# Optimization experiments

Measured on AMD Instinct MI355X. Metric: run time of the kernel, lower is better.

## Reference

```python
import jax, jax.numpy as jnp
import numpy as np

B, T, D, K, DEPTH = 8, 1024, 128, 64, 1


def _rel_ids(T, k):
    # relative_mat_id[i, j] = clamp(k + j - i, 0, 2k)
    base = jnp.arange(k, k + T)[None, :] - jnp.arange(T)[:, None]
    return jnp.clip(base, 0, 2 * k)  # [T, T] int32


def setup_inputs() -> dict:
    key = jax.random.key(0)
    ks = jax.random.split(key, 13)
    s = 1.0 / np.sqrt(D)
    return {
        "x": jax.random.normal(ks[0], (B, T, D), dtype=jnp.float32),
        "W0": jax.random.normal(ks[1], (D, D), dtype=jnp.float32) * s,
        "b0": jnp.zeros((D,), dtype=jnp.float32),
        "Wq": jax.random.normal(ks[2], (D, D), dtype=jnp.float32) * s,
        "bq": jnp.zeros((D,), dtype=jnp.float32),
        "Wk": jax.random.normal(ks[3], (D, D), dtype=jnp.float32) * s,
        "bk": jnp.zeros((D,), dtype=jnp.float32),
        "Wv": jax.random.normal(ks[4], (D, D), dtype=jnp.float32) * s,
        "bv": jnp.zeros((D,), dtype=jnp.float32),
        "W1": jax.random.normal(ks[5], (D, D), dtype=jnp.float32) * s,
        "b1": jnp.zeros((D,), dtype=jnp.float32),
        "pe_key": jax.random.normal(ks[6], (2 * K + 1, D), dtype=jnp.float32) * np.sqrt(2.0 / (2 * K + 1)),
        "pe_value": jax.random.normal(ks[7], (2 * K + 1, D), dtype=jnp.float32) * np.sqrt(2.0 / (2 * K + 1)),
    }


def reference(x, W0, b0, Wq, bq, Wk, bk, Wv, bv, W1, b1, pe_key, pe_value):
    Tlen = x.shape[1]
    ids = _rel_ids(Tlen, K)                     # [T, T]
    rpr_key = pe_key[ids]                       # [T, T, D]
    rpr_value = pe_value[ids]                   # [T, T, D]

    hs = jax.nn.relu(x @ W0 + b0)               # fc0 (dropout = eval identity)
    for _ in range(DEPTH):
        q = jnp.tanh(hs @ Wq + bq)
        k = jnp.tanh(hs @ Wk + bk)
        v = jnp.tanh(hs @ Wv + bv)
        a = jnp.einsum("bid,bjd->bij", q, k)
        a = a + jnp.einsum("ijd,bid->bij", rpr_key, q)
        a = jax.nn.softmax(a, axis=2)
        c = jnp.einsum("bij,bjd->bid", a, v)
        c = c + jnp.einsum("bij,ijd->bid", a, rpr_value)
        hs = jax.nn.relu(c @ W1 + b1)
    return hs
```

## Files before the change

### kernel.cpp

```cpp
#include <hip/hip_runtime.h>


#define TT 1024
#define DD 128
#define NB 8
#define SJH 1160

typedef _Float16 f16;
typedef __attribute__((ext_vector_type(8))) _Float16 f16x8;
typedef __attribute__((ext_vector_type(4))) _Float16 f16x4;
typedef __attribute__((ext_vector_type(4))) float f32x4;

static __device__ inline float fast_tanh(float x) {
    float xc = fminf(fmaxf(x, -12.f), 12.f);
    float e = __expf(2.f * xc);
    return (e - 1.f) / (e + 1.f);
}

__global__ __launch_bounds__(256) void prep_misc(
        const float* __restrict__ W0, const float* __restrict__ Wq,
        const float* __restrict__ Wk, const float* __restrict__ Wv,
        const float* __restrict__ W1, const float* __restrict__ PEK,
        const float* __restrict__ PEV, f16* __restrict__ wt,
        char* __restrict__ pekimg, char* __restrict__ pevimg) {
    const int blk = blockIdx.x, t = threadIdx.x;
    if (blk < 5) {
        const float* W = blk == 0 ? W0 : blk == 1 ? Wq : blk == 2 ? Wk
                       : blk == 3 ? Wv : W1;
        f16* o = wt + (size_t)blk * 16384;
        for (int it = 0; it < 64; it++) {
            int idx = t + 256 * it;
            int n = idx >> 7, k2 = idx & 127;
            o[n * 128 + k2] = (f16)W[k2 * 128 + n];
        }
    } else if (blk == 5) {
        for (int it = 0; it < 64; it++) {
            int idx = t + 256 * it;
            int m = idx >> 7, d = idx & 127;
            char* dst = pekimg + (m >> 6) * 16384 + (m & 63) * 256
                      + ((2 * d) ^ ((m & 7) << 4));
            *(f16*)dst = (f16)PEK[m * 128 + d];
        }
    } else if (blk == 6) {
        for (int it = 0; it < 64; it++) {
            int idx = t + 256 * it;
            int m = idx >> 7, d = idx & 127;
            char* dst = pevimg + (m >> 6) * 16384 + d * 128
                      + ((2 * (m & 63)) ^ ((d & 7) << 4));
            *(f16*)dst = (f16)PEV[m * 128 + d];
        }
    }
}

template<int ACT, int INF32, int OUTF32>
__global__ __launch_bounds__(256) void gemm16(const void* __restrict__ Xv,
        const f16* __restrict__ WT, const float* __restrict__ Bv,
        void* __restrict__ Yv) {
    __shared__ __align__(16) char lds[40960];
    char* xs = lds;
    char* wl = lds + 8192;
    const int t = threadIdx.x, wv = t >> 6, l = t & 63;
    const int r0 = blockIdx.x * 32;

    {
        const char* src = (const char*)WT;
        #pragma unroll
        for (int i = 0; i < 8; i++) {
            int a = t * 128 + i * 16;
            uint4 d = *(const uint4*)(src + a);
            *(uint4*)(wl + (a ^ (((a >> 8) & 7) << 4))) = d;
        }
    }
    if (INF32) {
        const float* X = (const float*)Xv + (size_t)r0 * 128;
        #pragma unroll
        for (int i = 0; i < 2; i++) {
            f32x4 a0 = *(const f32x4*)(X + t * 16 + i * 8);
            f32x4 a1 = *(const f32x4*)(X + t * 16 + i * 8 + 4);
            f16x8 h;
            h[0]=(f16)a0[0]; h[1]=(f16)a0[1]; h[2]=(f16)a0[2]; h[3]=(f16)a0[3];
            h[4]=(f16)a1[0]; h[5]=(f16)a1[1]; h[6]=(f16)a1[2]; h[7]=(f16)a1[3];
            int a = t * 32 + i * 16;
            *(f16x8*)(xs + (a ^ (((a >> 8) & 7) << 4))) = h;
        }
    } else {
        const char* X = (const char*)Xv + (size_t)r0 * 256;
        #pragma unroll
        for (int i = 0; i < 2; i++) {
            int a = t * 32 + i * 16;
            uint4 d = *(const uint4*)(X + a);
            *(uint4*)(xs + (a ^ (((a >> 8) & 7) << 4))) = d;
        }
    }
    __syncthreads();

    f32x4 acc[2][2] = {};
    #pragma unroll
    for (int c = 0; c < 4; c++) {
        f16x8 af[2], bf[2];
        #pragma unroll
        for (int it = 0; it < 2; it++) {
            int row = it * 16 + (l & 15);
            int a = (row << 8) + (c << 6) + ((l >> 4) << 4);
            af[it] = *(const f16x8*)(xs + (a ^ ((row & 7) << 4)));
        }
        #pragma unroll
        for (int nt = 0; nt < 2; nt++) {
            int n = wv * 32 + nt * 16 + (l & 15);
            int a = (n << 8) + (c << 6) + ((l >> 4) << 4);
            bf[nt] = *(const f16x8*)(wl + (a ^ ((n & 7) << 4)));
        }
        #pragma unroll
        for (int it = 0; it < 2; it++)
            #pragma unroll
            for (int nt = 0; nt < 2; nt++)
                acc[it][nt] = __builtin_amdgcn_mfma_f32_16x16x32_f16(
                        af[it], bf[nt], acc[it][nt], 0, 0, 0);
    }

    #pragma unroll
    for (int it = 0; it < 2; it++)
        #pragma unroll
        for (int nt = 0; nt < 2; nt++) {
            int n = wv * 32 + nt * 16 + (l & 15);
            float bb = Bv[n];
            #pragma unroll
            for (int r = 0; r < 4; r++) {
                int i = it * 16 + (l >> 4) * 4 + r;
                float v = acc[it][nt][r] + bb;
                v = (ACT == 0) ? fmaxf(v, 0.f) : fast_tanh(v);
                if (OUTF32) ((float*)Yv)[(size_t)(r0 + i) * 128 + n] = v;
                else        ((f16*)Yv)[(size_t)(r0 + i) * 128 + n] = (f16)v;
            }
        }
}

__global__ __launch_bounds__(256) void gemm_qkv(const f16* __restrict__ X,
        const f16* __restrict__ wt, const float* __restrict__ bq,
        const float* __restrict__ bk, const float* __restrict__ bv,
        f16* __restrict__ q16, char* __restrict__ kimg, char* __restrict__ vimg) {
    __shared__ __align__(16) char lds[40960];
    char* xs = lds;
    char* wl = lds + 8192;
    const int t = threadIdx.x, wv = t >> 6, l = t & 63;
    const int sel = blockIdx.x % 3;
    const int r0 = (blockIdx.x / 3) * 32;
    const f16* WT = wt + (size_t)(sel + 1) * 16384;
    const float* Bv = sel == 0 ? bq : sel == 1 ? bk : bv;

    {
        const char* src = (const char*)WT;
        #pragma unroll
        for (int i = 0; i < 8; i++) {
            int a = t * 128 + i * 16;
            uint4 d = *(const uint4*)(src + a);
            *(uint4*)(wl + (a ^ (((a >> 8) & 7) << 4))) = d;
        }
    }
    {
        const char* Xc = (const char*)X + (size_t)r0 * 256;
        #pragma unroll
        for (int i = 0; i < 2; i++) {
            int a = t * 32 + i * 16;
            uint4 d = *(const uint4*)(Xc + a);
            *(uint4*)(xs + (a ^ (((a >> 8) & 7) << 4))) = d;
        }
    }
    __syncthreads();

    f32x4 acc[2][2] = {};
    #pragma unroll
    for (int c = 0; c < 4; c++) {
        f16x8 af[2], bf[2];
        #pragma unroll
        for (int it = 0; it < 2; it++) {
            int row = it * 16 + (l & 15);
            int a = (row << 8) + (c << 6) + ((l >> 4) << 4);
            af[it] = *(const f16x8*)(xs + (a ^ ((row & 7) << 4)));
        }
        #pragma unroll
        for (int nt = 0; nt < 2; nt++) {
            int n = wv * 32 + nt * 16 + (l & 15);
            int a = (n << 8) + (c << 6) + ((l >> 4) << 4);
            bf[nt] = *(const f16x8*)(wl + (a ^ ((n & 7) << 4)));
        }
        #pragma unroll
        for (int it = 0; it < 2; it++)
            #pragma unroll
            for (int nt = 0; nt < 2; nt++)
                acc[it][nt] = __builtin_amdgcn_mfma_f32_16x16x32_f16(
                        af[it], bf[nt], acc[it][nt], 0, 0, 0);
    }

    if (sel == 0) {
        #pragma unroll
        for (int it = 0; it < 2; it++)
            #pragma unroll
            for (int nt = 0; nt < 2; nt++) {
                int n = wv * 32 + nt * 16 + (l & 15);
                float bb = Bv[n];
                #pragma unroll
                for (int r = 0; r < 4; r++) {
                    int i = it * 16 + (l >> 4) * 4 + r;
                    q16[(size_t)(r0 + i) * 128 + n] = (f16)fast_tanh(acc[it][nt][r] + bb);
                }
            }
    } else if (sel == 1) {
        __syncthreads();
        f16* ts = (f16*)lds;
        #pragma unroll
        for (int it = 0; it < 2; it++)
            #pragma unroll
            for (int nt = 0; nt < 2; nt++) {
                int n = wv * 32 + nt * 16 + (l & 15);
                float bb = Bv[n];
                #pragma unroll
                for (int r = 0; r < 4; r++) {
                    int i = it * 16 + (l >> 4) * 4 + r;
                    ts[i * 128 + n] = (f16)fast_tanh(acc[it][nt][r] + bb);
                }
            }
        __syncthreads();
        #pragma unroll
        for (int half = 0; half < 2; half++) {
            int row = (t >> 4) + half * 16, seg = t & 15;
            int jg = r0 + row, jp = jg & 63;
            char* dst = kimg + (size_t)((jg >> 10) * 16 + ((jg & 1023) >> 6)) * 16384
                      + jp * 256 + ((seg * 16) ^ ((jp & 7) << 4));
            *(f16x8*)dst = *(const f16x8*)&ts[row * 128 + seg * 8];
        }
    } else {
        #pragma unroll
        for (int it = 0; it < 2; it++)
            #pragma unroll
            for (int nt = 0; nt < 2; nt++) {
                int n = wv * 32 + nt * 16 + (l & 15);
                float bb = Bv[n];
                f16x4 h;
                #pragma unroll
                for (int r = 0; r < 4; r++)
                    h[r] = (f16)fast_tanh(acc[it][nt][r] + bb);
                int jb = r0 + it * 16 + ((l >> 4) << 2);
                char* dst = vimg + (size_t)((jb >> 10) * 16 + ((jb & 1023) >> 6)) * 16384
                          + n * 128 + ((2 * (jb & 63)) ^ ((n & 7) << 4));
                *(f16x4*)dst = h;
            }
    }
}

#define ISSUE(src, bi) do {                                                      \
    const char* _g = (src) + t * 16;                                             \
    char* _d = BUF + (bi) * 16384 + t * 16;                                      \
    __builtin_amdgcn_global_load_lds(                                            \
        (const __attribute__((address_space(1))) unsigned*)_g,                   \
        (__attribute__((address_space(3))) unsigned*)_d, 16, 0, 0);              \
    __builtin_amdgcn_global_load_lds(                                            \
        (const __attribute__((address_space(1))) unsigned*)(_g + 8192),          \
        (__attribute__((address_space(3))) unsigned*)(_d + 8192), 16, 0, 0);     \
} while (0)

__global__ __launch_bounds__(512) void attn_v5(
        const f16* __restrict__ q16, const char* __restrict__ kimg,
        const char* __restrict__ pekimg, const char* __restrict__ vimg,
        const char* __restrict__ pevimg, const float* __restrict__ PEK,
        const float* __restrict__ PEV, f16* __restrict__ c16) {
    extern __shared__ __align__(16) char sm5[];
    f16*   S   = (f16*)sm5;
    char*  BUF = sm5 + 74240;
    f16*   QB  = (f16*)(sm5 + 74240 + 65536);
    float* LR  = (float*)(sm5 + 74240 + 65536 + 8448);

    const int t = threadIdx.x, wv = t >> 6, l = t & 63;
    const int lr = l & 15, lg = l >> 4;
    const int b = blockIdx.x & 7;
    const int i0 = (blockIdx.x >> 3) << 5;
    const int it = wv & 1, jsub = wv >> 1;

    f16x8 qf[4];
    {
        const f16* qb = q16 + (size_t)(b * 1024 + i0 + it * 16 + lr) * 128 + lg * 8;
        #pragma unroll
        for (int c = 0; c < 4; c++) qf[c] = *(const f16x8*)(qb + c * 32);
    }

    const char* kbase = kimg + (size_t)b * 16 * 16384;
    const char* vbase = vimg + (size_t)b * 16 * 16384;

    ISSUE(kbase, 0);
    ISSUE(kbase + 16384, 1);

    for (int ch = 0; ch < 18; ch++) {
        if (ch < 14)      ISSUE(kbase + (size_t)(ch + 2) * 16384, (ch + 2) & 3);
        else if (ch < 16) ISSUE(pekimg + (size_t)(ch - 14) * 16384, (ch + 2) & 3);
        else              ISSUE(vbase + (size_t)(ch - 16) * 16384, (ch + 2) & 3);
        asm volatile("s_waitcnt vmcnt(4)" ::: "memory");
        __builtin_amdgcn_s_barrier();
        __builtin_amdgcn_sched_barrier(0);

        const char* kb = BUF + (ch & 3) * 16384;
        const int jp = jsub * 16 + lr;
        f32x4 acc = {0.f, 0.f, 0.f, 0.f};
        #pragma unroll
        for (int c = 0; c < 4; c++) {
            f16x8 kf = *(const f16x8*)(kb + jp * 256 + ((c * 64 + lg * 16) ^ ((jp & 7) << 4)));
            acc = __builtin_amdgcn_mfma_f32_16x16x32_f16(kf, qf[c], acc, 0, 0, 0);
        }
        f16x4 h = {(f16)acc[0], (f16)acc[1], (f16)acc[2], (f16)acc[3]};
        *(f16x4*)&S[(it * 16 + lr) * SJH + ch * 64 + jsub * 16 + lg * 4] = h;
    }
    asm volatile("s_waitcnt lgkmcnt(0)" ::: "memory");
    __builtin_amdgcn_s_barrier();
    __builtin_amdgcn_sched_barrier(0);

    {
        const int row = t >> 4, l16 = t & 15;
        const int ig = i0 + row;
        f16* srow = S + row * SJH;
        f16* qrow = QB + row * 132;

        float qp;
        {
            const f16* qr = q16 + (size_t)(b * 1024 + ig) * 128 + l16 * 8;
            const float* pr = PEK + 128 * 128 + l16 * 8;
            f16x8 qv = *(const f16x8*)qr;
            float s = 0.f;
            #pragma unroll
            for (int e = 0; e < 8; e++) s += (float)qv[e] * pr[e];
            #pragma unroll
            for (int off = 8; off; off >>= 1) s += __shfl_xor(s, off, 64);
            qp = s;
        }
        for (int mm = l16; mm < 128; mm += 16) {
            qrow[mm] = srow[1024 + mm];
            srow[1024 + mm] = (f16)0.f;
        }
        if (l16 == 0) qrow[128] = (f16)qp;
        const float qlo = (float)qrow[0], qhi = qp;

        float lmax = -3.0e38f;
        #pragma unroll
        for (int kk = 0; kk < 8; kk++) {
            int j0 = kk * 128 + l16 * 8;
            f16x8 sv = *(const f16x8*)(srow + j0);
            #pragma unroll
            for (int e = 0; e < 8; e++) {
                int idd = 64 + j0 + e - ig;
                float qv = (idd <= 0) ? qlo : (idd >= 128 ? qhi : (float)qrow[idd]);
                lmax = fmaxf(lmax, (float)sv[e] + qv);
            }
        }
        #pragma unroll
        for (int off = 8; off; off >>= 1) lmax = fmaxf(lmax, __shfl_xor(lmax, off, 64));

        float lsum = 0.f, s0 = 0.f, s1 = 0.f;
        #pragma unroll
        for (int kk = 0; kk < 8; kk++) {
            int j0 = kk * 128 + l16 * 8;
            f16x8 sv = *(const f16x8*)(srow + j0);
            f16x8 pv;
            #pragma unroll
            for (int e = 0; e < 8; e++) {
                int idd = 64 + j0 + e - ig;
                float qv = (idd <= 0) ? qlo : (idd >= 128 ? qhi : (float)qrow[idd]);
                float p = __expf((float)sv[e] + qv - lmax);
                pv[e] = (f16)p;
                lsum += p;
                if (idd <= 0)        s0 += p;
                else if (idd >= 128) s1 += p;
                else                 srow[1024 + idd] = (f16)p;
            }
            *(f16x8*)(srow + j0) = pv;
        }
        #pragma unroll
        for (int off = 8; off; off >>= 1) {
            lsum += __shfl_xor(lsum, off, 64);
            s0   += __shfl_xor(s0,   off, 64);
            s1   += __shfl_xor(s1,   off, 64);
        }
        if (l16 == 0) {
            srow[1024] = (f16)s0;
            srow[1152] = (f16)s1;
            LR[row] = lsum;
        }
    }
    asm volatile("s_waitcnt lgkmcnt(0)" ::: "memory");
    __builtin_amdgcn_s_barrier();
    __builtin_amdgcn_sched_barrier(0);

    f32x4 cacc[2] = {};
    for (int ch = 0; ch < 18; ch++) {
        if (ch < 14) {
            ISSUE(vbase + (size_t)(ch + 2) * 16384, (ch + 4) & 3);
            asm volatile("s_waitcnt vmcnt(4)" ::: "memory");
        } else if (ch < 16) {
            ISSUE(pevimg + (size_t)(ch - 14) * 16384, (ch + 4) & 3);
            asm volatile("s_waitcnt vmcnt(4)" ::: "memory");
        } else if (ch == 16) {
            asm volatile("s_waitcnt vmcnt(2)" ::: "memory");
        } else {
            asm volatile("s_waitcnt vmcnt(0)" ::: "memory");
        }
        __builtin_amdgcn_s_barrier();
        __builtin_amdgcn_sched_barrier(0);

        const char* vb = BUF + ((ch + 2) & 3) * 16384;
        const int dp = wv * 16 + lr;
        #pragma unroll
        for (int c2 = 0; c2 < 2; c2++) {
            f16x8 vf = *(const f16x8*)(vb + dp * 128 + ((c2 * 64 + lg * 16) ^ ((dp & 7) << 4)));
            #pragma unroll
            for (int i2 = 0; i2 < 2; i2++) {
                f16x8 pf = *(const f16x8*)&S[(i2 * 16 + lr) * SJH + ch * 64 + c2 * 32 + lg * 8];
                cacc[i2] = __builtin_amdgcn_mfma_f32_16x16x32_f16(vf, pf, cacc[i2], 0, 0, 0);
            }
        }
    }

    #pragma unroll
    for (int i2 = 0; i2 < 2; i2++) {
        const int irow = i2 * 16 + lr;
        const float w128 = (float)S[irow * SJH + 1152];
        const float rin = 1.f / LR[irow];
        const float* pvr = PEV + 128 * 128;
        f16x4 h;
        #pragma unroll
        for (int r = 0; r < 4; r++) {
            int d = wv * 16 + lg * 4 + r;
            h[r] = (f16)((cacc[i2][r] + w128 * pvr[d]) * rin);
        }
        *(f16x4*)(c16 + (size_t)(b * 1024 + i0 + irow) * 128 + wv * 16 + lg * 4) = h;
    }
}


extern "C" void kernel_launch(void* const* d_in, const int* in_sizes, int n_in,
                              void* d_out, int out_size, void* d_ws, size_t ws_size,
                              hipStream_t stream) {
    const float* x   = (const float*)d_in[0];
    const float* W0  = (const float*)d_in[1];
    const float* b0  = (const float*)d_in[2];
    const float* Wq  = (const float*)d_in[3];
    const float* bq  = (const float*)d_in[4];
    const float* Wk  = (const float*)d_in[5];
    const float* bk  = (const float*)d_in[6];
    const float* Wv  = (const float*)d_in[7];
    const float* bv  = (const float*)d_in[8];
    const float* W1  = (const float*)d_in[9];
    const float* b1  = (const float*)d_in[10];
    const float* pek = (const float*)d_in[11];
    const float* pev = (const float*)d_in[12];
    float* out = (float*)d_out;

    const size_t NTD = (size_t)NB * TT * DD;
    f16* hs16 = (f16*)d_ws;
    f16* q16  = hs16 + NTD;
    f16* c16  = q16 + NTD;
    f16* wt   = c16 + NTD;
    char* kimg   = (char*)(wt + 5 * 16384);
    char* vimg   = kimg + (size_t)8 * 16 * 16384;
    char* pekimg = vimg + (size_t)8 * 16 * 16384;
    char* pevimg = pekimg + 32768;

    const int SMEM_ATTN = 74240 + 65536 + 8448 + 128;
    hipFuncSetAttribute(reinterpret_cast<const void*>(attn_v5),
                        hipFuncAttributeMaxDynamicSharedMemorySize, SMEM_ATTN);

    hipLaunchKernelGGL(prep_misc, dim3(7), dim3(256), 0, stream,
                       W0, Wq, Wk, Wv, W1, pek, pev, wt, pekimg, pevimg);
    hipLaunchKernelGGL((gemm16<0,1,0>), dim3(256), dim3(256), 0, stream,
                       x, wt, b0, hs16);
    hipLaunchKernelGGL(gemm_qkv, dim3(768), dim3(256), 0, stream,
                       hs16, wt, bq, bk, bv, q16, kimg, vimg);
    hipLaunchKernelGGL(attn_v5, dim3(256), dim3(512), SMEM_ATTN, stream,
                       q16, kimg, pekimg, vimg, pevimg, pek, pev, c16);
    hipLaunchKernelGGL((gemm16<0,0,1>), dim3(256), dim3(256), 0, stream,
                       c16, wt + 4 * 16384, b1, out);
}
```

Before: 57.98 us.

## Fuse fc0 into QKV kernel and fc1 into attention, use 128-row K/V chunks

The fc0 GEMM is folded into a single kernel that keeps the relu'd hidden state in LDS and computes Q, K and V from it, so the hs16 round trip through global memory and one launch are gone. The W1 output projection plus relu is fused into the attention epilogue, which removes the c16 buffer and the final GEMM launch. The K/V image layout moves to 128-row 32KB chunks with double buffering and full vmcnt(0) waits, replacing the 4-deep 16KB pipeline. The trade-off is more serial work per block (four dependent GEMMs in the QKV kernel, 258 blocks instead of 768) and shallower load prefetch in attention.

```diff
diff --git a/kernel.cpp b/kernel.cpp
--- a/kernel.cpp
+++ b/kernel.cpp
@@ -17,62 +17,83 @@
     return (e - 1.f) / (e + 1.f);
 }
 
-__global__ __launch_bounds__(256) void prep_misc(
+__global__ __launch_bounds__(256) void prep_w(
         const float* __restrict__ W0, const float* __restrict__ Wq,
         const float* __restrict__ Wk, const float* __restrict__ Wv,
-        const float* __restrict__ W1, const float* __restrict__ PEK,
-        const float* __restrict__ PEV, f16* __restrict__ wt,
-        char* __restrict__ pekimg, char* __restrict__ pevimg) {
+        const float* __restrict__ W1, f16* __restrict__ wt) {
     const int blk = blockIdx.x, t = threadIdx.x;
-    if (blk < 5) {
-        const float* W = blk == 0 ? W0 : blk == 1 ? Wq : blk == 2 ? Wk
-                       : blk == 3 ? Wv : W1;
-        f16* o = wt + (size_t)blk * 16384;
-        for (int it = 0; it < 64; it++) {
-            int idx = t + 256 * it;
-            int n = idx >> 7, k2 = idx & 127;
-            o[n * 128 + k2] = (f16)W[k2 * 128 + n];
-        }
-    } else if (blk == 5) {
-        for (int it = 0; it < 64; it++) {
-            int idx = t + 256 * it;
-            int m = idx >> 7, d = idx & 127;
-            char* dst = pekimg + (m >> 6) * 16384 + (m & 63) * 256
-                      + ((2 * d) ^ ((m & 7) << 4));
-            *(f16*)dst = (f16)PEK[m * 128 + d];
-        }
-    } else if (blk == 6) {
-        for (int it = 0; it < 64; it++) {
-            int idx = t + 256 * it;
-            int m = idx >> 7, d = idx & 127;
-            char* dst = pevimg + (m >> 6) * 16384 + d * 128
-                      + ((2 * (m & 63)) ^ ((d & 7) << 4));
-            *(f16*)dst = (f16)PEV[m * 128 + d];
-        }
+    const float* W = blk == 0 ? W0 : blk == 1 ? Wq : blk == 2 ? Wk
+                   : blk == 3 ? Wv : W1;
+    f16* o = wt + (size_t)blk * 16384;
+    for (int it = 0; it < 64; it++) {
+        int idx = t + 256 * it;
+        int n = idx >> 7, k2 = idx & 127;
+        o[n * 128 + k2] = (f16)W[k2 * 128 + n];
     }
 }
 
-template<int ACT, int INF32, int OUTF32>
-__global__ __launch_bounds__(256) void gemm16(const void* __restrict__ Xv,
-        const f16* __restrict__ WT, const float* __restrict__ Bv,
-        void* __restrict__ Yv) {
-    __shared__ __align__(16) char lds[40960];
-    char* xs = lds;
-    char* wl = lds + 8192;
+#define STAGEW(s) do { const char* _src = (const char*)(wt + (size_t)(s) * 16384); \
+    _Pragma("unroll") for (int _i = 0; _i < 8; _i++) { \
+        int _a = t * 128 + _i * 16; uint4 _d = *(const uint4*)(_src + _a); \
+        *(uint4*)(wl + (_a ^ (((_a >> 8) & 7) << 4))) = _d; } } while (0)
+
+#define ZACC() do { _Pragma("unroll") for (int _i = 0; _i < 2; _i++) \
+    _Pragma("unroll") for (int _j = 0; _j < 2; _j++) \
+        acc[_i][_j] = (f32x4){0.f, 0.f, 0.f, 0.f}; } while (0)
+
+#define GEMMCORE(SRC) do { \
+    _Pragma("unroll") for (int _c = 0; _c < 4; _c++) { \
+        f16x8 _af[2], _bf[2]; \
+        _Pragma("unroll") for (int _it = 0; _it < 2; _it++) { \
+            int _row = _it * 16 + (l & 15); \
+            int _a = (_row << 8) + (_c << 6) + ((l >> 4) << 4); \
+            _af[_it] = *(const f16x8*)((SRC) + (_a ^ ((_row & 7) << 4))); } \
+        _Pragma("unroll") for (int _nt = 0; _nt < 2; _nt++) { \
+            int _n = wv * 32 + _nt * 16 + (l & 15); \
+            int _a = (_n << 8) + (_c << 6) + ((l >> 4) << 4); \
+            _bf[_nt] = *(const f16x8*)(wl + (_a ^ ((_n & 7) << 4))); } \
+        _Pragma("unroll") for (int _it = 0; _it < 2; _it++) \
+        _Pragma("unroll") for (int _nt = 0; _nt < 2; _nt++) \
+            acc[_it][_nt] = __builtin_amdgcn_mfma_f32_16x16x32_f16( \
+                    _af[_it], _bf[_nt], acc[_it][_nt], 0, 0, 0); } } while (0)
+
+__global__ __launch_bounds__(256) void fused_qkv(
+        const float* __restrict__ x, const f16* __restrict__ wt,
+        const float* __restrict__ b0, const float* __restrict__ bq,
+        const float* __restrict__ bk, const float* __restrict__ bv,
+        const float* __restrict__ PEK, const float* __restrict__ PEV,
+        f16* __restrict__ q16, char* __restrict__ kimg,
+        char* __restrict__ vimg, char* __restrict__ pekimg,
+        char* __restrict__ pevimg) {
+    __shared__ __align__(16) char lds[49152];
+    char* xs  = lds;
+    char* hsl = lds + 8192;
+    char* wl  = lds + 16384;
     const int t = threadIdx.x, wv = t >> 6, l = t & 63;
-    const int r0 = blockIdx.x * 32;
-
-    {
-        const char* src = (const char*)WT;
-        #pragma unroll
-        for (int i = 0; i < 8; i++) {
-            int a = t * 128 + i * 16;
-            uint4 d = *(const uint4*)(src + a);
-            *(uint4*)(wl + (a ^ (((a >> 8) & 7) << 4))) = d;
-        }
-    }
-    if (INF32) {
-        const float* X = (const float*)Xv + (size_t)r0 * 128;
+    const int blk = blockIdx.x;
+
+    if (blk >= 256) {
+        if (blk == 256) {
+            for (int it = 0; it < 64; it++) {
+                int idx = t + 256 * it;
+                int m = idx >> 7, d = idx & 127;
+                *(f16*)(pekimg + m * 256 + ((2 * d) ^ ((m & 7) << 4))) =
+                        (f16)PEK[m * 128 + d];
+            }
+        } else {
+            for (int it = 0; it < 64; it++) {
+                int idx = t + 256 * it;
+                int m = idx >> 7, d = idx & 127;
+                *(f16*)(pevimg + d * 256 + ((2 * m) ^ ((d & 7) << 4))) =
+                        (f16)PEV[m * 128 + d];
+            }
+        }
+        return;
+    }
+
+    const int r0 = blk * 32;
+    {
+        const float* X = x + (size_t)r0 * 128;
         #pragma unroll
         for (int i = 0; i < 2; i++) {
             f32x4 a0 = *(const f32x4*)(X + t * 16 + i * 8);
@@ -83,234 +104,172 @@
             int a = t * 32 + i * 16;
             *(f16x8*)(xs + (a ^ (((a >> 8) & 7) << 4))) = h;
         }
-    } else {
-        const char* X = (const char*)Xv + (size_t)r0 * 256;
-        #pragma unroll
-        for (int i = 0; i < 2; i++) {
-            int a = t * 32 + i * 16;
-            uint4 d = *(const uint4*)(X + a);
-            *(uint4*)(xs + (a ^ (((a >> 8) & 7) << 4))) = d;
-        }
-    }
-    __syncthreads();
-
-    f32x4 acc[2][2] = {};
-    #pragma unroll
-    for (int c = 0; c < 4; c++) {
-        f16x8 af[2], bf[2];
-        #pragma unroll
-        for (int it = 0; it < 2; it++) {
-            int row = it * 16 + (l & 15);
-            int a = (row << 8) + (c << 6) + ((l >> 4) << 4);
-            af[it] = *(const f16x8*)(xs + (a ^ ((row & 7) << 4)));
-        }
-        #pragma unroll
-        for (int nt = 0; nt < 2; nt++) {
-            int n = wv * 32 + nt * 16 + (l & 15);
-            int a = (n << 8) + (c << 6) + ((l >> 4) << 4);
-            bf[nt] = *(const f16x8*)(wl + (a ^ ((n & 7) << 4)));
-        }
-        #pragma unroll
-        for (int it = 0; it < 2; it++)
-            #pragma unroll
-            for (int nt = 0; nt < 2; nt++)
-                acc[it][nt] = __builtin_amdgcn_mfma_f32_16x16x32_f16(
-                        af[it], bf[nt], acc[it][nt], 0, 0, 0);
-    }
-
-    #pragma unroll
-    for (int it = 0; it < 2; it++)
-        #pragma unroll
-        for (int nt = 0; nt < 2; nt++) {
-            int n = wv * 32 + nt * 16 + (l & 15);
-            float bb = Bv[n];
-            #pragma unroll
-            for (int r = 0; r < 4; r++) {
-                int i = it * 16 + (l >> 4) * 4 + r;
-                float v = acc[it][nt][r] + bb;
-                v = (ACT == 0) ? fmaxf(v, 0.f) : fast_tanh(v);
-                if (OUTF32) ((float*)Yv)[(size_t)(r0 + i) * 128 + n] = v;
-                else        ((f16*)Yv)[(size_t)(r0 + i) * 128 + n] = (f16)v;
-            }
-        }
-}
-
-__global__ __launch_bounds__(256) void gemm_qkv(const f16* __restrict__ X,
-        const f16* __restrict__ wt, const float* __restrict__ bq,
-        const float* __restrict__ bk, const float* __restrict__ bv,
-        f16* __restrict__ q16, char* __restrict__ kimg, char* __restrict__ vimg) {
-    __shared__ __align__(16) char lds[40960];
-    char* xs = lds;
-    char* wl = lds + 8192;
-    const int t = threadIdx.x, wv = t >> 6, l = t & 63;
-    const int sel = blockIdx.x % 3;
-    const int r0 = (blockIdx.x / 3) * 32;
-    const f16* WT = wt + (size_t)(sel + 1) * 16384;
-    const float* Bv = sel == 0 ? bq : sel == 1 ? bk : bv;
-
-    {
-        const char* src = (const char*)WT;
-        #pragma unroll
-        for (int i = 0; i < 8; i++) {
-            int a = t * 128 + i * 16;
-            uint4 d = *(const uint4*)(src + a);
-            *(uint4*)(wl + (a ^ (((a >> 8) & 7) << 4))) = d;
-        }
-    }
-    {
-        const char* Xc = (const char*)X + (size_t)r0 * 256;
-        #pragma unroll
-        for (int i = 0; i < 2; i++) {
-            int a = t * 32 + i * 16;
-            uint4 d = *(const uint4*)(Xc + a);
-            *(uint4*)(xs + (a ^ (((a >> 8) & 7) << 4))) = d;
-        }
-    }
-    __syncthreads();
-
-    f32x4 acc[2][2] = {};
-    #pragma unroll
-    for (int c = 0; c < 4; c++) {
-        f16x8 af[2], bf[2];
-        #pragma unroll
-        for (int it = 0; it < 2; it++) {
-            int row = it * 16 + (l & 15);
-            int a = (row << 8) + (c << 6) + ((l >> 4) << 4);
-            af[it] = *(const f16x8*)(xs + (a ^ ((row & 7) << 4)));
-        }
-        #pragma unroll
-        for (int nt = 0; nt < 2; nt++) {
-            int n = wv * 32 + nt * 16 + (l & 15);
-            int a = (n << 8) + (c << 6) + ((l >> 4) << 4);
-            bf[nt] = *(const f16x8*)(wl + (a ^ ((n & 7) << 4)));
-        }
-        #pragma unroll
-        for (int it = 0; it < 2; it++)
-            #pragma unroll
-            for (int nt = 0; nt < 2; nt++)
-                acc[it][nt] = __builtin_amdgcn_mfma_f32_16x16x32_f16(
-                        af[it], bf[nt], acc[it][nt], 0, 0, 0);
-    }
-
-    if (sel == 0) {
+    }
+    STAGEW(0);
+    __syncthreads();
+
+    f32x4 acc[2][2];
+    ZACC();
+    GEMMCORE(xs);
+    __syncthreads();
+    {
         #pragma unroll
         for (int it = 0; it < 2; it++)
             #pragma unroll
             for (int nt = 0; nt < 2; nt++) {
                 int n = wv * 32 + nt * 16 + (l & 15);
-                float bb = Bv[n];
+                float bb = b0[n];
                 #pragma unroll
                 for (int r = 0; r < 4; r++) {
                     int i = it * 16 + (l >> 4) * 4 + r;
-                    q16[(size_t)(r0 + i) * 128 + n] = (f16)fast_tanh(acc[it][nt][r] + bb);
+                    float v = fmaxf(acc[it][nt][r] + bb, 0.f);
+                    int a = i * 256 + 2 * n;
+                    *(f16*)(hsl + (a ^ ((i & 7) << 4))) = (f16)v;
                 }
             }
-    } else if (sel == 1) {
-        __syncthreads();
-        f16* ts = (f16*)lds;
+    }
+    STAGEW(1);
+    __syncthreads();
+
+    ZACC();
+    GEMMCORE(hsl);
+    {
         #pragma unroll
         for (int it = 0; it < 2; it++)
             #pragma unroll
             for (int nt = 0; nt < 2; nt++) {
                 int n = wv * 32 + nt * 16 + (l & 15);
-                float bb = Bv[n];
+                float bb = bq[n];
+                #pragma unroll
+                for (int r = 0; r < 4; r++) {
+                    int i = it * 16 + (l >> 4) * 4 + r;
+                    q16[(size_t)(r0 + i) * 128 + n] =
+                            (f16)fast_tanh(acc[it][nt][r] + bb);
+                }
+            }
+    }
+    __syncthreads();
+    STAGEW(2);
+    __syncthreads();
+
+    ZACC();
+    GEMMCORE(hsl);
+    __syncthreads();
+    f16* ts = (f16*)xs;
+    {
+        #pragma unroll
+        for (int it = 0; it < 2; it++)
+            #pragma unroll
+            for (int nt = 0; nt < 2; nt++) {
+                int n = wv * 32 + nt * 16 + (l & 15);
+                float bb = bk[n];
                 #pragma unroll
                 for (int r = 0; r < 4; r++) {
                     int i = it * 16 + (l >> 4) * 4 + r;
                     ts[i * 128 + n] = (f16)fast_tanh(acc[it][nt][r] + bb);
                 }
             }
-        __syncthreads();
+    }
+    STAGEW(3);
+    __syncthreads();
+    {
         #pragma unroll
         for (int half = 0; half < 2; half++) {
-            int row = (t >> 4) + half * 16, seg = t & 15;
-            int jg = r0 + row, jp = jg & 63;
-            char* dst = kimg + (size_t)((jg >> 10) * 16 + ((jg & 1023) >> 6)) * 16384
-                      + jp * 256 + ((seg * 16) ^ ((jp & 7) << 4));
+            int row = (t >> 4) + half * 16;
+            int seg = t & 15;
+            int jg = r0 + row;
+            int chunk = ((jg >> 10) << 3) + ((jg & 1023) >> 7);
+            int jp = jg & 127;
+            char* dst = kimg + (size_t)chunk * 32768 + jp * 256
+                      + ((seg * 16) ^ ((jp & 7) << 4));
             *(f16x8*)dst = *(const f16x8*)&ts[row * 128 + seg * 8];
         }
-    } else {
+    }
+    ZACC();
+    GEMMCORE(hsl);
+    {
         #pragma unroll
         for (int it = 0; it < 2; it++)
             #pragma unroll
             for (int nt = 0; nt < 2; nt++) {
-                int n = wv * 32 + nt * 16 + (l & 15);
-                float bb = Bv[n];
+                int d = wv * 32 + nt * 16 + (l & 15);
+                float bb = bv[d];
                 f16x4 h;
                 #pragma unroll
                 for (int r = 0; r < 4; r++)
                     h[r] = (f16)fast_tanh(acc[it][nt][r] + bb);
                 int jb = r0 + it * 16 + ((l >> 4) << 2);
-                char* dst = vimg + (size_t)((jb >> 10) * 16 + ((jb & 1023) >> 6)) * 16384
-                          + n * 128 + ((2 * (jb & 63)) ^ ((n & 7) << 4));
+                int chunk = ((jb >> 10) << 3) + ((jb & 1023) >> 7);
+                char* dst = vimg + (size_t)chunk * 32768 + d * 256
+                          + ((2 * (jb & 127)) ^ ((d & 7) << 4));
                 *(f16x4*)dst = h;
             }
     }
 }
 
-#define ISSUE(src, bi) do {                                                      \
-    const char* _g = (src) + t * 16;                                             \
-    char* _d = BUF + (bi) * 16384 + t * 16;                                      \
-    __builtin_amdgcn_global_load_lds(                                            \
-        (const __attribute__((address_space(1))) unsigned*)_g,                   \
-        (__attribute__((address_space(3))) unsigned*)_d, 16, 0, 0);              \
-    __builtin_amdgcn_global_load_lds(                                            \
-        (const __attribute__((address_space(1))) unsigned*)(_g + 8192),          \
-        (__attribute__((address_space(3))) unsigned*)(_d + 8192), 16, 0, 0);     \
+#define ISSUE32(src, bi) do { const char* _g = (src) + t * 16; \
+    char* _d = BUF + (bi) * 32768 + t * 16; \
+    _Pragma("unroll") for (int _i = 0; _i < 4; _i++) \
+        __builtin_amdgcn_global_load_lds( \
+            (const __attribute__((address_space(1))) unsigned*)(_g + _i * 8192), \
+            (__attribute__((address_space(3))) unsigned*)(_d + _i * 8192), 16, 0, 0); \
 } while (0)
 
-__global__ __launch_bounds__(512) void attn_v5(
+__global__ __launch_bounds__(512) void attn_all(
         const f16* __restrict__ q16, const char* __restrict__ kimg,
         const char* __restrict__ pekimg, const char* __restrict__ vimg,
         const char* __restrict__ pevimg, const float* __restrict__ PEK,
-        const float* __restrict__ PEV, f16* __restrict__ c16) {
-    extern __shared__ __align__(16) char sm5[];
-    f16*   S   = (f16*)sm5;
-    char*  BUF = sm5 + 74240;
-    f16*   QB  = (f16*)(sm5 + 74240 + 65536);
-    float* LR  = (float*)(sm5 + 74240 + 65536 + 8448);
+        const float* __restrict__ PEV, const f16* __restrict__ w1t,
+        const float* __restrict__ b1, float* __restrict__ out) {
+    extern __shared__ __align__(16) char sm6[];
+    f16*   S   = (f16*)sm6;
+    char*  BUF = sm6 + 74240;
+    f16*   QB  = (f16*)(sm6 + 74240 + 65536);
+    float* LR  = (float*)(sm6 + 74240 + 65536 + 8448);
 
     const int t = threadIdx.x, wv = t >> 6, l = t & 63;
     const int lr = l & 15, lg = l >> 4;
     const int b = blockIdx.x & 7;
     const int i0 = (blockIdx.x >> 3) << 5;
-    const int it = wv & 1, jsub = wv >> 1;
+    const int it16 = (wv & 1) << 4;
+    const int jsub = wv >> 1;
 
     f16x8 qf[4];
     {
-        const f16* qb = q16 + (size_t)(b * 1024 + i0 + it * 16 + lr) * 128 + lg * 8;
+        const f16* qb = q16 + (size_t)(b * TT + i0 + it16 + lr) * 128 + lg * 8;
         #pragma unroll
         for (int c = 0; c < 4; c++) qf[c] = *(const f16x8*)(qb + c * 32);
     }
 
-    const char* kbase = kimg + (size_t)b * 16 * 16384;
-    const char* vbase = vimg + (size_t)b * 16 * 16384;
-
-    ISSUE(kbase, 0);
-    ISSUE(kbase + 16384, 1);
-
-    for (int ch = 0; ch < 18; ch++) {
-        if (ch < 14)      ISSUE(kbase + (size_t)(ch + 2) * 16384, (ch + 2) & 3);
-        else if (ch < 16) ISSUE(pekimg + (size_t)(ch - 14) * 16384, (ch + 2) & 3);
-        else              ISSUE(vbase + (size_t)(ch - 16) * 16384, (ch + 2) & 3);
-        asm volatile("s_waitcnt vmcnt(4)" ::: "memory");
+    const char* kbase = kimg + (size_t)b * 8 * 32768;
+    const char* vbase = vimg + (size_t)b * 8 * 32768;
+
+    ISSUE32(kbase, 0);
+    for (int ch = 0; ch < 9; ++ch) {
+        asm volatile("s_waitcnt vmcnt(0)" ::: "memory");
         __builtin_amdgcn_s_barrier();
         __builtin_amdgcn_sched_barrier(0);
-
-        const char* kb = BUF + (ch & 3) * 16384;
-        const int jp = jsub * 16 + lr;
-        f32x4 acc = {0.f, 0.f, 0.f, 0.f};
-        #pragma unroll
-        for (int c = 0; c < 4; c++) {
-            f16x8 kf = *(const f16x8*)(kb + jp * 256 + ((c * 64 + lg * 16) ^ ((jp & 7) << 4)));
-            acc = __builtin_amdgcn_mfma_f32_16x16x32_f16(kf, qf[c], acc, 0, 0, 0);
-        }
-        f16x4 h = {(f16)acc[0], (f16)acc[1], (f16)acc[2], (f16)acc[3]};
-        *(f16x4*)&S[(it * 16 + lr) * SJH + ch * 64 + jsub * 16 + lg * 4] = h;
+        if (ch < 8)
+            ISSUE32(ch < 7 ? kbase + (size_t)(ch + 1) * 32768 : pekimg, (ch + 1) & 1);
+        const char* kb = BUF + (ch & 1) * 32768;
+        #pragma unroll
+        for (int jt = 0; jt < 2; jt++) {
+            const int jp = jsub * 32 + jt * 16 + lr;
+            f32x4 acc = {0.f, 0.f, 0.f, 0.f};
+            #pragma unroll
+            for (int c = 0; c < 4; c++) {
+                f16x8 kf = *(const f16x8*)(kb + jp * 256
+                            + ((c * 64 + lg * 16) ^ ((jp & 7) << 4)));
+                acc = __builtin_amdgcn_mfma_f32_16x16x32_f16(kf, qf[c], acc, 0, 0, 0);
+            }
+            f16x4 h = {(f16)acc[0], (f16)acc[1], (f16)acc[2], (f16)acc[3]};
+            *(f16x4*)&S[(it16 + lr) * SJH + ch * 128 + jsub * 32 + jt * 16 + lg * 4] = h;
+        }
     }
     asm volatile("s_waitcnt lgkmcnt(0)" ::: "memory");
     __builtin_amdgcn_s_barrier();
     __builtin_amdgcn_sched_barrier(0);
+    ISSUE32(vbase, 0);
 
     {
         const int row = t >> 4, l16 = t & 15;
@@ -320,7 +279,7 @@
 
         float qp;
         {
-            const f16* qr = q16 + (size_t)(b * 1024 + ig) * 128 + l16 * 8;
+            const f16* qr = q16 + (size_t)(b * TT + ig) * 128 + l16 * 8;
             const float* pr = PEK + 128 * 128 + l16 * 8;
             f16x8 qv = *(const f16x8*)qr;
             float s = 0.f;
@@ -388,47 +347,92 @@
     __builtin_amdgcn_sched_barrier(0);
 
     f32x4 cacc[2] = {};
-    for (int ch = 0; ch < 18; ch++) {
-        if (ch < 14) {
-            ISSUE(vbase + (size_t)(ch + 2) * 16384, (ch + 4) & 3);
-            asm volatile("s_waitcnt vmcnt(4)" ::: "memory");
-        } else if (ch < 16) {
-            ISSUE(pevimg + (size_t)(ch - 14) * 16384, (ch + 4) & 3);
-            asm volatile("s_waitcnt vmcnt(4)" ::: "memory");
-        } else if (ch == 16) {
-            asm volatile("s_waitcnt vmcnt(2)" ::: "memory");
-        } else {
-            asm volatile("s_waitcnt vmcnt(0)" ::: "memory");
-        }
+    for (int ch = 0; ch < 9; ++ch) {
+        asm volatile("s_waitcnt vmcnt(0)" ::: "memory");
         __builtin_amdgcn_s_barrier();
         __builtin_amdgcn_sched_barrier(0);
-
-        const char* vb = BUF + ((ch + 2) & 3) * 16384;
+        if (ch < 8)
+            ISSUE32(ch < 7 ? vbase + (size_t)(ch + 1) * 32768 : pevimg, (ch + 1) & 1);
+        const char* vb = BUF + (ch & 1) * 32768;
         const int dp = wv * 16 + lr;
         #pragma unroll
-        for (int c2 = 0; c2 < 2; c2++) {
-            f16x8 vf = *(const f16x8*)(vb + dp * 128 + ((c2 * 64 + lg * 16) ^ ((dp & 7) << 4)));
+        for (int c2 = 0; c2 < 4; c2++) {
+            f16x8 vf = *(const f16x8*)(vb + dp * 256
+                        + ((c2 * 64 + lg * 16) ^ ((dp & 7) << 4)));
             #pragma unroll
             for (int i2 = 0; i2 < 2; i2++) {
-                f16x8 pf = *(const f16x8*)&S[(i2 * 16 + lr) * SJH + ch * 64 + c2 * 32 + lg * 8];
+                f16x8 pf = *(const f16x8*)&S[(i2 * 16 + lr) * SJH
+                            + ch * 128 + c2 * 32 + lg * 8];
                 cacc[i2] = __builtin_amdgcn_mfma_f32_16x16x32_f16(vf, pf, cacc[i2], 0, 0, 0);
             }
         }
     }
 
+    float w128[2], rden[2];
     #pragma unroll
     for (int i2 = 0; i2 < 2; i2++) {
-        const int irow = i2 * 16 + lr;
-        const float w128 = (float)S[irow * SJH + 1152];
-        const float rin = 1.f / LR[irow];
+        int irow = i2 * 16 + lr;
+        w128[i2] = (float)S[irow * SJH + 1152];
+        rden[i2] = 1.f / LR[irow];
+    }
+    __syncthreads();
+    char* cl = (char*)S;
+    {
         const float* pvr = PEV + 128 * 128;
-        f16x4 h;
-        #pragma unroll
-        for (int r = 0; r < 4; r++) {
-            int d = wv * 16 + lg * 4 + r;
-            h[r] = (f16)((cacc[i2][r] + w128 * pvr[d]) * rin);
-        }
-        *(f16x4*)(c16 + (size_t)(b * 1024 + i0 + irow) * 128 + wv * 16 + lg * 4) = h;
+        #pragma unroll
+        for (int i2 = 0; i2 < 2; i2++) {
+            int i = i2 * 16 + lr;
+            #pragma unroll
+            for (int r = 0; r < 4; r++) {
+                int d = wv * 16 + lg * 4 + r;
+                float cv = (cacc[i2][r] + w128[i2] * pvr[d]) * rden[i2];
+                int a = i * 256 + 2 * d;
+                *(f16*)(cl + (a ^ ((i & 7) << 4))) = (f16)cv;
+            }
+        }
+    }
+    char* wl4 = BUF;
+    {
+        const char* src = (const char*)w1t;
+        #pragma unroll
+        for (int i = 0; i < 4; i++) {
+            int a = t * 64 + i * 16;
+            uint4 dta = *(const uint4*)(src + a);
+            *(uint4*)(wl4 + (a ^ (((a >> 8) & 7) << 4))) = dta;
+        }
+    }
+    __syncthreads();
+
+    f32x4 oacc[2] = {};
+    #pragma unroll
+    for (int c = 0; c < 4; c++) {
+        f16x8 af[2], bf;
+        #pragma unroll
+        for (int i2 = 0; i2 < 2; i2++) {
+            int row = i2 * 16 + lr;
+            int a = (row << 8) + (c << 6) + (lg << 4);
+            af[i2] = *(const f16x8*)(cl + (a ^ ((row & 7) << 4)));
+        }
+        {
+            int n = wv * 16 + lr;
+            int a = (n << 8) + (c << 6) + (lg << 4);
+            bf = *(const f16x8*)(wl4 + (a ^ ((n & 7) << 4)));
+        }
+        #pragma unroll
+        for (int i2 = 0; i2 < 2; i2++)
+            oacc[i2] = __builtin_amdgcn_mfma_f32_16x16x32_f16(af[i2], bf, oacc[i2], 0, 0, 0);
+    }
+    {
+        int n = wv * 16 + lr;
+        float bb = b1[n];
+        #pragma unroll
+        for (int i2 = 0; i2 < 2; i2++) {
+            #pragma unroll
+            for (int r = 0; r < 4; r++) {
+                int i = i2 * 16 + lg * 4 + r;
+                out[(size_t)(b * TT + i0 + i) * DD + n] = fmaxf(oacc[i2][r] + bb, 0.f);
+            }
+        }
     }
 }
 
@@ -452,27 +456,23 @@
     float* out = (float*)d_out;
 
     const size_t NTD = (size_t)NB * TT * DD;
-    f16* hs16 = (f16*)d_ws;
-    f16* q16  = hs16 + NTD;
-    f16* c16  = q16 + NTD;
-    f16* wt   = c16 + NTD;
+    f16* q16 = (f16*)d_ws;
+    f16* wt  = q16 + NTD;
     char* kimg   = (char*)(wt + 5 * 16384);
-    char* vimg   = kimg + (size_t)8 * 16 * 16384;
-    char* pekimg = vimg + (size_t)8 * 16 * 16384;
+    char* vimg   = kimg + (size_t)64 * 32768;
+    char* pekimg = vimg + (size_t)64 * 32768;
     char* pevimg = pekimg + 32768;
 
     const int SMEM_ATTN = 74240 + 65536 + 8448 + 128;
-    hipFuncSetAttribute(reinterpret_cast<const void*>(attn_v5),
+    hipFuncSetAttribute(reinterpret_cast<const void*>(attn_all),
                         hipFuncAttributeMaxDynamicSharedMemorySize, SMEM_ATTN);
 
-    hipLaunchKernelGGL(prep_misc, dim3(7), dim3(256), 0, stream,
-                       W0, Wq, Wk, Wv, W1, pek, pev, wt, pekimg, pevimg);
-    hipLaunchKernelGGL((gemm16<0,1,0>), dim3(256), dim3(256), 0, stream,
-                       x, wt, b0, hs16);
-    hipLaunchKernelGGL(gemm_qkv, dim3(768), dim3(256), 0, stream,
-                       hs16, wt, bq, bk, bv, q16, kimg, vimg);
-    hipLaunchKernelGGL(attn_v5, dim3(256), dim3(512), SMEM_ATTN, stream,
-                       q16, kimg, pekimg, vimg, pevimg, pek, pev, c16);
-    hipLaunchKernelGGL((gemm16<0,0,1>), dim3(256), dim3(256), 0, stream,
-                       c16, wt + 4 * 16384, b1, out);
+    hipLaunchKernelGGL(prep_w, dim3(5), dim3(256), 0, stream,
+                       W0, Wq, Wk, Wv, W1, wt);
+    hipLaunchKernelGGL(fused_qkv, dim3(258), dim3(256), 0, stream,
+                       x, wt, b0, bq, bk, bv, pek, pev,
+                       q16, kimg, vimg, pekimg, pevimg);
+    hipLaunchKernelGGL(attn_all, dim3(256), dim3(512), SMEM_ATTN, stream,
+                       q16, kimg, pekimg, vimg, pevimg, pek, pev,
+                       wt + 4 * 16384, b1, out);
 }
```

Measured after the change: 56.49 us. -2.6%, faster.
